# Performance work log

Measured on AMD Instinct MI355X. Metric: run time of the kernel, lower is better.

The kernel has to match this reference:

```python
import jax, jax.numpy as jnp
import numpy as np

TEMPERATURE = 0.07
MARGIN = 0.2
EPS = 1e-8  # matches torch F.cosine_similarity eps


def _cosine_matrix(a, b):
    # a: (N, D), b: (M, D) -> (N, M) pairwise cosine similarity
    an = a / jnp.clip(jnp.linalg.norm(a, axis=-1, keepdims=True), EPS)
    bn = b / jnp.clip(jnp.linalg.norm(b, axis=-1, keepdims=True), EPS)
    return an @ bn.T


def setup_inputs() -> dict:
    key = jax.random.key(0)
    k1, k2, k3 = jax.random.split(key, 3)
    return {
        "step_embeddings": jax.random.normal(k1, (8192, 1024), dtype=jnp.float32),
        "modal_embeddings": jax.random.normal(k2, (4096, 1024), dtype=jnp.float32),
        "negative_modal_embeddings": jax.random.normal(k3, (4096, 1024), dtype=jnp.float32),
    }


def reference(step_embeddings, modal_embeddings, negative_modal_embeddings):
    # --- step-modal alignment (max cosine sim per step, averaged) ---
    S = _cosine_matrix(step_embeddings, modal_embeddings)        # (N, M)
    per_step = S.max(axis=1)                                      # (N,)
    alignment = per_step.mean()

    # --- attention-weighted alignment (use_attention=True) ---
    logits = (step_embeddings @ modal_embeddings.T) / TEMPERATURE  # (N, M)
    attention = jax.nn.softmax(logits, axis=1)
    weighted_alignment = (S * attention).sum(axis=1).mean()

    # --- contrastive coherence against negatives ---
    Sn = _cosine_matrix(step_embeddings, negative_modal_embeddings)
    negative_alignment = Sn.max(axis=1).mean()
    positive_alignment = alignment
    contrastive_score = positive_alignment - negative_alignment
    margin_score = jax.nn.relu(contrastive_score - MARGIN)

    # --- per-step coherence (same max-cosine per step) ---
    min_step_coherence = per_step.min()

    # overall uses weighted_alignment (attention on), mixed with contrastive
    overall = 0.7 * weighted_alignment + 0.3 * contrastive_score

    return (alignment, weighted_alignment, attention, contrastive_score,
            margin_score, positive_alignment, negative_alignment,
            per_step, min_step_coherence, overall)
```

## Files before the change

### kernel.cpp

```cpp
#include <hip/hip_runtime.h>
#include <cmath>


#define WAVE 64

typedef __bf16 bf16x8_t __attribute__((ext_vector_type(8)));
typedef __bf16 bf16x4_t __attribute__((ext_vector_type(4)));
typedef float f32x4_t __attribute__((ext_vector_type(4)));

__device__ __forceinline__ float wave_reduce_sum(float v) {
#pragma unroll
    for (int o = 32; o > 0; o >>= 1) v += __shfl_down(v, o, WAVE);
    return v;
}
__device__ __forceinline__ float wave_reduce_max(float v) {
#pragma unroll
    for (int o = 32; o > 0; o >>= 1) v = fmaxf(v, __shfl_down(v, o, WAVE));
    return v;
}
__device__ __forceinline__ float wave_reduce_min(float v) {
#pragma unroll
    for (int o = 32; o > 0; o >>= 1) v = fminf(v, __shfl_down(v, o, WAVE));
    return v;
}

__device__ __forceinline__ unsigned enc_f(float f) {
    unsigned u = __float_as_uint(f);
    return (u & 0x80000000u) ? ~u : (u | 0x80000000u);
}
__device__ __forceinline__ float dec_f(unsigned e) {
    unsigned u = (e & 0x80000000u) ? (e & 0x7fffffffu) : ~e;
    return __uint_as_float(u);
}

__global__ __launch_bounds__(256)
void convert_norms_kernel(const float* __restrict__ step,
                          const float* __restrict__ modal,
                          const float* __restrict__ negs,
                          char* __restrict__ arena,
                          float* __restrict__ ina, float* __restrict__ inb,
                          float* __restrict__ inn,
                          unsigned* __restrict__ negmax_u, int N, int M) {
    const int tid = threadIdx.x, lane = tid & 63, wv = tid >> 6;
    const int b = blockIdx.x * 4 + wv;
    const float* src;
    if (b < N)          src = step  + (size_t)b * 1024;
    else if (b < N + M) src = modal + (size_t)(b - N) * 1024;
    else                src = negs  + (size_t)(b - N - M) * 1024;

    char* cb = arena + (((size_t)(b >> 2)) << 14) + ((size_t)(b & 3) << 11) + 8192;
    float s = 0.0f;
#pragma unroll
    for (int q = 0; q < 4; q++) {
        const int idx = lane + q * 64;
        const float4 v = ((const float4*)src)[idx];
        bf16x4_t o;
        o[0] = (__bf16)v.x; o[1] = (__bf16)v.y;
        o[2] = (__bf16)v.z; o[3] = (__bf16)v.w;
        *(bf16x4_t*)(cb + (size_t)idx * 8) = o;
        s += v.x * v.x + v.y * v.y + v.z * v.z + v.w * v.w;
    }
    s = wave_reduce_sum(s);
    if (lane == 0) {
        const float inv = 1.0f / fmaxf(sqrtf(s), 1e-8f);
        if (b < N)          { ina[b] = inv; negmax_u[b] = 0u; }
        else if (b < N + M) inb[b - N] = inv;
        else                inn[b - N - M] = inv;
    }
}

#define GLD16(g, l)                                                       \
    __builtin_amdgcn_global_load_lds(                                     \
        (const __attribute__((address_space(1))) void*)(g),               \
        (__attribute__((address_space(3))) void*)(l), 16, 0, 0)

#define BAR()   asm volatile("s_barrier" ::: "memory")
#define LGKM0() asm volatile("s_waitcnt lgkmcnt(0)" ::: "memory")
#define VMW(n)  asm volatile("s_waitcnt vmcnt(" #n ")" ::: "memory")

#define STAGE_A(Ab, kt)                                                   \
    _Pragma("unroll")                                                     \
    for (int h = 0; h < 2; h++)                                           \
    _Pragma("unroll")                                                     \
      for (int c = 0; c < 2; c++)                                         \
        GLD16(arena + srcA[h][c] + (size_t)(kt) * 128,                    \
              (Ab) + h * 8192 + c * 4096 + w * 512);

#define STAGE_B(Bb, kt)                                                   \
    _Pragma("unroll")                                                     \
    for (int h = 0; h < 2; h++)                                           \
    _Pragma("unroll")                                                     \
      for (int c = 0; c < 2; c++)                                         \
        GLD16(arena + srcB[h][c] + (size_t)(kt) * 128,                    \
              (Bb) + h * 8192 + c * 4096 + w * 512);

#define READ_A(g, Ab)                                                     \
    _Pragma("unroll")                                                     \
    for (int ii = 0; ii < 4; ii++)                                        \
    _Pragma("unroll")                                                     \
      for (int kk = 0; kk < 2; kk++)                                      \
        af[ii][kk] = *(const bf16x8_t*)&(Ab)[arow0 + (g) * 4096 +         \
                                             ii * 1024 + koff[kk]];

#define READ_B(j0, dst, Bb)                                               \
    _Pragma("unroll")                                                     \
    for (int jj = 0; jj < 2; jj++)                                        \
    _Pragma("unroll")                                                     \
      for (int kk = 0; kk < 2; kk++)                                      \
        dst[jj][kk] = *(const bf16x8_t*)&(Bb)[brow0 + ((j0) + jj) * 1024 +\
                                              koff[kk]];

#define READ_B01(Bb) READ_B(0, bf01, Bb)
#define READ_B23(Bb) READ_B(2, bf23, Bb)

#define MFMA_Q(i0, j0, bsrc)                                              \
    __builtin_amdgcn_s_setprio(1);                                        \
    _Pragma("unroll")                                                     \
    for (int kk = 0; kk < 2; kk++)                                        \
    _Pragma("unroll")                                                     \
      for (int ii = 0; ii < 4; ii++)                                      \
      _Pragma("unroll")                                                   \
        for (int jj = 0; jj < 2; jj++)                                    \
          acc[(i0) + ii][(j0) + jj] =                                     \
              __builtin_amdgcn_mfma_f32_16x16x32_bf16(                    \
                  af[ii][kk], bsrc[jj][kk], acc[(i0) + ii][(j0) + jj],    \
                  0, 0, 0);                                               \
    __builtin_amdgcn_s_setprio(0);

#define TILE(Ac, Bc, An, Bn, ktpre, pre, rd)                              \
    LGKM0();                     \
    MFMA_Q(0, 0, bf01);                                                   \
    READ_B23(Bc);                           \
    LGKM0();                                                              \
    MFMA_Q(0, 2, bf23);                                                   \
    READ_A(1, Ac);          \
    BAR();                        \
    if (pre) { STAGE_B(Bc, ktpre); }                                      \
    LGKM0();                                             \
    MFMA_Q(4, 0, bf01);                                                   \
    BAR();                        \
    if (pre) { STAGE_A(Ac, ktpre); }                                      \
    MFMA_Q(4, 2, bf23);                                                   \
    if (rd) {                                                             \
        if (pre) { VMW(8); } else { VMW(0); }                             \
        BAR();                      \
        READ_A(0, An);           \
        READ_B01(Bn);                                                     \
    }

__global__ __launch_bounds__(512, 2)
void gemm_fused_kernel(char* __restrict__ arena, int N, int M,
                       const float* __restrict__ inv_nn,
                       unsigned* __restrict__ negmax_u) {
    __shared__ __bf16 As[2][256 * 64];
    __shared__ __bf16 Bs[2][256 * 64];

    const int lin = blockIdx.x;
    const int xcd = lin & 7;
    const int j   = lin >> 3;
    const int r   = j >> 5;
    const int u   = j & 31;
    const int bm = ((xcd << 2) + (u & 3)) << 8;
    const int bn = ((r << 3) + (u >> 2)) << 8;

    const int t = threadIdx.x, w = t >> 6, lane = t & 63;
    const int lane16 = lane & 15, lq = lane >> 4;
    const int wm = w >> 2, wn = w & 3;

    const int l3 = lane >> 3, ol = lane & 7;
    const int og = ol ^ l3;
    unsigned srcA[2][2], srcB[2][2];
#pragma unroll
    for (int h = 0; h < 2; h++)
#pragma unroll
      for (int c = 0; c < 2; c++) {
        const int ga = bm + h * 128 + c * 64 + w * 8 + l3;
        srcA[h][c] = ((unsigned)(ga >> 2) << 14) + ((unsigned)(ga & 3) << 11)
                     + 8192u + (unsigned)og * 16u;
        const int gb = N + bn + h * 128 + c * 64 + w * 8 + l3;
        srcB[h][c] = ((unsigned)(gb >> 2) << 14) + ((unsigned)(gb & 3) << 11)
                     + 8192u + (unsigned)og * 16u;
      }

    const int sxr = lane16 & 7;
    int koff[2];
#pragma unroll
    for (int kk = 0; kk < 2; kk++) koff[kk] = ((lq + 4 * kk) ^ sxr) * 8;
    const int arow0 = wm * 8192 + lane16 * 64;
    const int brow0 = wn * 4096 + lane16 * 64;

    f32x4_t acc[8][4];
#pragma unroll
    for (int i = 0; i < 8; i++)
#pragma unroll
      for (int j2 = 0; j2 < 4; j2++) acc[i][j2] = (f32x4_t){0.f, 0.f, 0.f, 0.f};

    bf16x8_t af[4][2], bf01[2][2], bf23[2][2];

    __bf16* const A0 = As[0]; __bf16* const A1 = As[1];
    __bf16* const B0 = Bs[0]; __bf16* const B1 = Bs[1];

    STAGE_A(A0, 0); STAGE_B(B0, 0);
    STAGE_A(A1, 1); STAGE_B(B1, 1);
    VMW(8);
    BAR();
    READ_A(0, A0);
    READ_B01(B0);

    for (int it = 0; it < 8; ++it) {
        const int pre = (it < 7);
        const int k2 = 2 * it + 2, k3 = 2 * it + 3;
        TILE(A0, B0, A1, B1, k2, pre, 1)
        TILE(A1, B1, A0, B0, k3, pre, pre)
    }

    if (bn < M) {
#pragma unroll
        for (int i = 0; i < 8; i++) {
#pragma unroll
            for (int rr = 0; rr < 4; rr++) {
                const int grow = bm + wm * 128 + i * 16 + lq * 4 + rr;
                __bf16* dst = (__bf16*)(arena + ((size_t)grow << 14)) +
                              bn + wn * 64 + lane16;
#pragma unroll
                for (int jj = 0; jj < 4; jj++)
                    dst[jj * 16] = (__bf16)acc[i][jj][rr];
            }
        }
    } else {
        float invn[4];
#pragma unroll
        for (int jj = 0; jj < 4; jj++)
            invn[jj] = inv_nn[(bn - M) + wn * 64 + jj * 16 + lane16];
#pragma unroll
        for (int i = 0; i < 8; i++) {
#pragma unroll
            for (int rr = 0; rr < 4; rr++) {
                float v = acc[i][0][rr] * invn[0];
                v = fmaxf(v, acc[i][1][rr] * invn[1]);
                v = fmaxf(v, acc[i][2][rr] * invn[2]);
                v = fmaxf(v, acc[i][3][rr] * invn[3]);
#pragma unroll
                for (int o = 8; o > 0; o >>= 1)
                    v = fmaxf(v, __shfl_xor(v, o, WAVE));
                if (lane16 == 0)
                    atomicMax(&negmax_u[bm + wm * 128 + i * 16 + lq * 4 + rr],
                              enc_f(v));
            }
        }
    }
}

#define CUT 2.0f
#define MAXCAND 64

__global__ __launch_bounds__(256)
void softmax_fix_kernel(char* __restrict__ arena, const float* __restrict__ step,
                        const float* __restrict__ modal,
                        const float* __restrict__ ina, const float* __restrict__ inb,
                        float* __restrict__ perstep, float* __restrict__ wout,
                        float* __restrict__ attn) {
    const int row = blockIdx.x, tid = threadIdx.x;
    const int lane = tid & 63, wv = tid >> 6;

    __shared__ float srow_s[1024];
    __shared__ float red[8];
    __shared__ float bcast[2];
    __shared__ int   cand[MAXCAND];
    __shared__ float exact[MAXCAND];
    __shared__ int   cnt;

    if (tid == 0) cnt = 0;
    ((float4*)srow_s)[tid] = ((const float4*)(step + (size_t)row * 1024))[tid];

    const __bf16* gb = (const __bf16*)(arena + ((size_t)row << 14));
    float vals[16];
    float invn[16];
#pragma unroll
    for (int g = 0; g < 4; g++) {
        const bf16x4_t v = *(const bf16x4_t*)(gb + g * 1024 + tid * 4);
        const float4 x = *(const float4*)(inb + g * 1024 + tid * 4);
        vals[g * 4 + 0] = (float)v[0]; vals[g * 4 + 1] = (float)v[1];
        vals[g * 4 + 2] = (float)v[2]; vals[g * 4 + 3] = (float)v[3];
        invn[g * 4 + 0] = x.x; invn[g * 4 + 1] = x.y;
        invn[g * 4 + 2] = x.z; invn[g * 4 + 3] = x.w;
    }

    float dmax = -3.4e38f;
#pragma unroll
    for (int j = 0; j < 16; j++) dmax = fmaxf(dmax, vals[j]);
    float wm = wave_reduce_max(dmax);
    if (lane == 0) red[wv] = wm;
    __syncthreads();
    if (tid == 0) bcast[0] = fmaxf(fmaxf(red[0], red[1]), fmaxf(red[2], red[3]));
    __syncthreads();
    const float m0 = bcast[0];

    const float thr = m0 - CUT;
#pragma unroll
    for (int g = 0; g < 4; g++)
#pragma unroll
        for (int u = 0; u < 4; u++) {
            if (vals[g * 4 + u] >= thr) {
                const int pos = atomicAdd(&cnt, 1);
                if (pos < MAXCAND) cand[pos] = g * 1024 + tid * 4 + u;
            }
        }
    __syncthreads();
    const int nc = min(cnt, MAXCAND);

    for (int i = wv; i < nc; i += 4) {
        const float* mrow = modal + (size_t)cand[i] * 1024;
        float p = 0.0f;
#pragma unroll
        for (int q = 0; q < 16; q++) {
            const int idx = lane + q * 64;
            p = fmaf(srow_s[idx], mrow[idx], p);
        }
        p = wave_reduce_sum(p);
        if (lane == 0) exact[i] = p;
    }
    __syncthreads();

    for (int i = 0; i < nc; i++) {
        const int c = cand[i];
        if (((c & 1023) >> 2) == tid) vals[(c >> 10) * 4 + (c & 3)] = exact[i];
    }

    float dmax2 = -3.4e38f, cmax = -3.4e38f;
#pragma unroll
    for (int j = 0; j < 16; j++) {
        dmax2 = fmaxf(dmax2, vals[j]);
        cmax = fmaxf(cmax, vals[j] * invn[j]);
    }
    float wg = wave_reduce_max(dmax2);
    float wc = wave_reduce_max(cmax);
    if (lane == 0) { red[wv] = wg; red[4 + wv] = wc; }
    __syncthreads();
    if (tid == 0) {
        bcast[0] = fmaxf(fmaxf(red[0], red[1]), fmaxf(red[2], red[3]));
        bcast[1] = fmaxf(fmaxf(red[4], red[5]), fmaxf(red[6], red[7]));
    }
    __syncthreads();
    const float invT = 1.0f / 0.07f;
    const float mlog = bcast[0] * invT;
    const float cmaxAll = bcast[1];

    float evals[16];
    float lsum = 0.0f;
#pragma unroll
    for (int j = 0; j < 16; j++) {
        const float e = __expf(vals[j] * invT - mlog);
        evals[j] = e;
        lsum += e;
    }
    lsum = wave_reduce_sum(lsum);
    __syncthreads();
    if (lane == 0) red[wv] = lsum;
    __syncthreads();
    if (tid == 0) bcast[0] = red[0] + red[1] + red[2] + red[3];
    __syncthreads();
    const float invZ = 1.0f / bcast[0];

    float* arow = attn + (size_t)row * 4096;
    float wacc = 0.0f;
#pragma unroll
    for (int g = 0; g < 4; g++) {
        float4 o;
        const float a0 = evals[g * 4 + 0] * invZ, a1 = evals[g * 4 + 1] * invZ;
        const float a2 = evals[g * 4 + 2] * invZ, a3 = evals[g * 4 + 3] * invZ;
        o.x = a0; o.y = a1; o.z = a2; o.w = a3;
        *(float4*)(arow + g * 1024 + tid * 4) = o;
        wacc += a0 * vals[g * 4 + 0] * invn[g * 4 + 0];
        wacc += a1 * vals[g * 4 + 1] * invn[g * 4 + 1];
        wacc += a2 * vals[g * 4 + 2] * invn[g * 4 + 2];
        wacc += a3 * vals[g * 4 + 3] * invn[g * 4 + 3];
    }
    wacc = wave_reduce_sum(wacc);
    __syncthreads();
    if (lane == 0) red[wv] = wacc;
    __syncthreads();
    if (tid == 0) {
        const float inv_na = ina[row];
        perstep[row] = cmaxAll * inv_na;
        wout[row] = (red[0] + red[1] + red[2] + red[3]) * inv_na;
    }
}

__global__ __launch_bounds__(1024)
void finalize_kernel(const float* __restrict__ perstep, const float* __restrict__ w,
                     const unsigned* __restrict__ negmax_u,
                     const float* __restrict__ ina, float* __restrict__ out,
                     int N, size_t NM) {
    float s_a = 0.0f, s_w = 0.0f, s_n = 0.0f, mn = 3.4e38f;
    for (int i = threadIdx.x; i < N; i += 1024) {
        const float p = perstep[i];
        s_a += p;
        s_w += w[i];
        s_n += dec_f(negmax_u[i]) * ina[i];
        mn = fminf(mn, p);
    }
    s_a = wave_reduce_sum(s_a);
    s_w = wave_reduce_sum(s_w);
    s_n = wave_reduce_sum(s_n);
    mn  = wave_reduce_min(mn);
    __shared__ float ra[16], rw[16], rn[16], rm[16];
    const int lane = threadIdx.x & 63, wv = threadIdx.x >> 6;
    if (lane == 0) { ra[wv] = s_a; rw[wv] = s_w; rn[wv] = s_n; rm[wv] = mn; }
    __syncthreads();
    if (threadIdx.x == 0) {
        float ta = 0, tw = 0, tn = 0, tm = 3.4e38f;
#pragma unroll
        for (int i = 0; i < 16; i++) {
            ta += ra[i]; tw += rw[i]; tn += rn[i]; tm = fminf(tm, rm[i]);
        }
        const float inv = 1.0f / (float)N;
        const float alignment = ta * inv;
        const float weighted  = tw * inv;
        const float neg       = tn * inv;
        const float contrast  = alignment - neg;
        const float margin    = fmaxf(contrast - 0.2f, 0.0f);
        const float overall   = 0.7f * weighted + 0.3f * contrast;
        out[0] = alignment;
        out[1] = weighted;
        float* p = out + 2 + NM;
        p[0] = contrast;
        p[1] = margin;
        p[2] = alignment;
        p[3] = neg;
        p[4 + N] = tm;
        p[5 + N] = overall;
    }
}

extern "C" void kernel_launch(void* const* d_in, const int* in_sizes, int n_in,
                              void* d_out, int out_size, void* d_ws, size_t ws_size,
                              hipStream_t stream) {
    const float* step  = (const float*)d_in[0];
    const float* modal = (const float*)d_in[1];
    const float* negs  = (const float*)d_in[2];
    float* out = (float*)d_out;

    const int K = 1024;
    const int N = in_sizes[0] / K;
    const int M = in_sizes[1] / K;
    const size_t NM = (size_t)N * (size_t)M;

    float* ina        = (float*)d_ws;
    float* inb        = ina + N;
    float* inn        = inb + M;
    unsigned* negmax  = (unsigned*)(inn + M);
    float* wsum       = (float*)(negmax + N);

    char* arena    = (char*)d_out + 16;
    float* attn    = out + 2;
    float* perstep = out + 2 + NM + 4;

    convert_norms_kernel<<<(N + 2 * M) / 4, 256, 0, stream>>>(
        step, modal, negs, arena, ina, inb, inn, negmax, N, M);

    const int nblocks = (N >> 8) * ((2 * M) >> 8);
    gemm_fused_kernel<<<nblocks, 512, 0, stream>>>(arena, N, M, inn, negmax);

    softmax_fix_kernel<<<N, 256, 0, stream>>>(arena, step, modal, ina, inb,
                                              perstep, wsum, attn);

    finalize_kernel<<<1, 1024, 0, stream>>>(perstep, wsum, negmax, ina, out, N, NM);
}
```

Measured before the change: 353.2 us.

## Reshape GEMM warp tiling to 64x128 and pipeline B fragment reads per quarter

Changes the per-wave output tile from 128x64 (2x4 wave grid) to 64x128 (4x2 grid), so each wave holds a single A fragment set and streams four B column chunks. The inner tile now double-buffers the B fragments with partial lgkmcnt waits and scheduling barriers so LDS reads overlap MFMAs. Global-to-LDS staging for the next k-tile is moved to after all MFMAs, between two barriers. The goal is fewer A fragment reloads and better overlap of LDS reads with compute, but the k-tile prefetch is now issued later, which leaves less time to hide global load latency.

```diff
diff --git a/kernel.cpp b/kernel.cpp
--- a/kernel.cpp
+++ b/kernel.cpp
@@ -74,9 +74,10 @@
         (const __attribute__((address_space(1))) void*)(g),               \
         (__attribute__((address_space(3))) void*)(l), 16, 0, 0)
 
-#define BAR()   asm volatile("s_barrier" ::: "memory")
-#define LGKM0() asm volatile("s_waitcnt lgkmcnt(0)" ::: "memory")
-#define VMW(n)  asm volatile("s_waitcnt vmcnt(" #n ")" ::: "memory")
+#define BAR()     asm volatile("s_barrier" ::: "memory")
+#define LGKMC(n)  asm volatile("s_waitcnt lgkmcnt(" #n ")" ::: "memory")
+#define VMW(n)    asm volatile("s_waitcnt vmcnt(" #n ")" ::: "memory")
+#define SB0()     __builtin_amdgcn_sched_barrier(0)
 
 #define STAGE_A(Ab, kt)                                                   \
     _Pragma("unroll")                                                     \
@@ -94,26 +95,23 @@
         GLD16(arena + srcB[h][c] + (size_t)(kt) * 128,                    \
               (Bb) + h * 8192 + c * 4096 + w * 512);
 
-#define READ_A(g, Ab)                                                     \
+#define READ_AF(Ab)                                                       \
     _Pragma("unroll")                                                     \
     for (int ii = 0; ii < 4; ii++)                                        \
     _Pragma("unroll")                                                     \
       for (int kk = 0; kk < 2; kk++)                                      \
-        af[ii][kk] = *(const bf16x8_t*)&(Ab)[arow0 + (g) * 4096 +         \
-                                             ii * 1024 + koff[kk]];
-
-#define READ_B(j0, dst, Bb)                                               \
+        af[ii][kk] = *(const bf16x8_t*)&(Ab)[arow0 + ii * 1024 +          \
+                                             koff[kk]];
+
+#define READ_BF(dst, c, Bb)                                               \
     _Pragma("unroll")                                                     \
     for (int jj = 0; jj < 2; jj++)                                        \
     _Pragma("unroll")                                                     \
       for (int kk = 0; kk < 2; kk++)                                      \
-        dst[jj][kk] = *(const bf16x8_t*)&(Bb)[brow0 + ((j0) + jj) * 1024 +\
-                                              koff[kk]];
-
-#define READ_B01(Bb) READ_B(0, bf01, Bb)
-#define READ_B23(Bb) READ_B(2, bf23, Bb)
-
-#define MFMA_Q(i0, j0, bsrc)                                              \
+        dst[jj][kk] = *(const bf16x8_t*)&(Bb)[brow0 + (c) * 2048 +        \
+                                              jj * 1024 + koff[kk]];
+
+#define MFMA_Q(c, bank)                                                   \
     __builtin_amdgcn_s_setprio(1);                                        \
     _Pragma("unroll")                                                     \
     for (int kk = 0; kk < 2; kk++)                                        \
@@ -121,31 +119,31 @@
       for (int ii = 0; ii < 4; ii++)                                      \
       _Pragma("unroll")                                                   \
         for (int jj = 0; jj < 2; jj++)                                    \
-          acc[(i0) + ii][(j0) + jj] =                                     \
+          acc[ii][(c) * 2 + jj] =                                         \
               __builtin_amdgcn_mfma_f32_16x16x32_bf16(                    \
-                  af[ii][kk], bsrc[jj][kk], acc[(i0) + ii][(j0) + jj],    \
+                  af[ii][kk], bank[jj][kk], acc[ii][(c) * 2 + jj],        \
                   0, 0, 0);                                               \
     __builtin_amdgcn_s_setprio(0);
 
 #define TILE(Ac, Bc, An, Bn, ktpre, pre, rd)                              \
-    LGKM0();                     \
-    MFMA_Q(0, 0, bf01);                                                   \
-    READ_B23(Bc);                           \
-    LGKM0();                                                              \
-    MFMA_Q(0, 2, bf23);                                                   \
-    READ_A(1, Ac);          \
-    BAR();                        \
-    if (pre) { STAGE_B(Bc, ktpre); }                                      \
-    LGKM0();                                             \
-    MFMA_Q(4, 0, bf01);                                                   \
-    BAR();                        \
-    if (pre) { STAGE_A(Ac, ktpre); }                                      \
-    MFMA_Q(4, 2, bf23);                                                   \
+    READ_BF(bfO, 1, Bc);                                                  \
+    LGKMC(4); SB0();                      \
+    MFMA_Q(0, bfE);                                                       \
+    READ_BF(bfE, 2, Bc);                                                  \
+    LGKMC(4); SB0();                         \
+    MFMA_Q(1, bfO);                                                       \
+    READ_BF(bfO, 3, Bc);                                                  \
+    LGKMC(4); SB0();                         \
+    MFMA_Q(2, bfE);                                                       \
+    LGKMC(0); SB0();                                        \
+    MFMA_Q(3, bfO);                                                       \
     if (rd) {                                                             \
-        if (pre) { VMW(8); } else { VMW(0); }                             \
-        BAR();                      \
-        READ_A(0, An);           \
-        READ_B01(Bn);                                                     \
+        BAR();                       \
+        if (pre) { STAGE_A(Ac, ktpre); STAGE_B(Bc, ktpre); VMW(8); }      \
+        else     { VMW(0); }                                              \
+        BAR();                                    \
+        READ_AF(An);                \
+        READ_BF(bfE, 0, Bn);                                              \
     }
 
 __global__ __launch_bounds__(512, 2)
@@ -165,7 +163,7 @@
 
     const int t = threadIdx.x, w = t >> 6, lane = t & 63;
     const int lane16 = lane & 15, lq = lane >> 4;
-    const int wm = w >> 2, wn = w & 3;
+    const int wm = w & 3, wn = w >> 2;
 
     const int l3 = lane >> 3, ol = lane & 7;
     const int og = ol ^ l3;
@@ -186,16 +184,16 @@
     int koff[2];
 #pragma unroll
     for (int kk = 0; kk < 2; kk++) koff[kk] = ((lq + 4 * kk) ^ sxr) * 8;
-    const int arow0 = wm * 8192 + lane16 * 64;
-    const int brow0 = wn * 4096 + lane16 * 64;
-
-    f32x4_t acc[8][4];
-#pragma unroll
-    for (int i = 0; i < 8; i++)
-#pragma unroll
-      for (int j2 = 0; j2 < 4; j2++) acc[i][j2] = (f32x4_t){0.f, 0.f, 0.f, 0.f};
-
-    bf16x8_t af[4][2], bf01[2][2], bf23[2][2];
+    const int arow0 = wm * 4096 + lane16 * 64;
+    const int brow0 = wn * 8192 + lane16 * 64;
+
+    f32x4_t acc[4][8];
+#pragma unroll
+    for (int i = 0; i < 4; i++)
+#pragma unroll
+      for (int j2 = 0; j2 < 8; j2++) acc[i][j2] = (f32x4_t){0.f, 0.f, 0.f, 0.f};
+
+    bf16x8_t af[4][2], bfE[2][2], bfO[2][2];
 
     __bf16* const A0 = As[0]; __bf16* const A1 = As[1];
     __bf16* const B0 = Bs[0]; __bf16* const B1 = Bs[1];
@@ -204,8 +202,8 @@
     STAGE_A(A1, 1); STAGE_B(B1, 1);
     VMW(8);
     BAR();
-    READ_A(0, A0);
-    READ_B01(B0);
+    READ_AF(A0);
+    READ_BF(bfE, 0, B0);
 
     for (int it = 0; it < 8; ++it) {
         const int pre = (it < 7);
@@ -216,35 +214,35 @@
 
     if (bn < M) {
 #pragma unroll
-        for (int i = 0; i < 8; i++) {
+        for (int i = 0; i < 4; i++) {
 #pragma unroll
             for (int rr = 0; rr < 4; rr++) {
-                const int grow = bm + wm * 128 + i * 16 + lq * 4 + rr;
+                const int grow = bm + wm * 64 + i * 16 + lq * 4 + rr;
                 __bf16* dst = (__bf16*)(arena + ((size_t)grow << 14)) +
-                              bn + wn * 64 + lane16;
-#pragma unroll
-                for (int jj = 0; jj < 4; jj++)
+                              bn + wn * 128 + lane16;
+#pragma unroll
+                for (int jj = 0; jj < 8; jj++)
                     dst[jj * 16] = (__bf16)acc[i][jj][rr];
             }
         }
     } else {
-        float invn[4];
-#pragma unroll
-        for (int jj = 0; jj < 4; jj++)
-            invn[jj] = inv_nn[(bn - M) + wn * 64 + jj * 16 + lane16];
-#pragma unroll
-        for (int i = 0; i < 8; i++) {
+        float invn[8];
+#pragma unroll
+        for (int jj = 0; jj < 8; jj++)
+            invn[jj] = inv_nn[(bn - M) + wn * 128 + jj * 16 + lane16];
+#pragma unroll
+        for (int i = 0; i < 4; i++) {
 #pragma unroll
             for (int rr = 0; rr < 4; rr++) {
                 float v = acc[i][0][rr] * invn[0];
-                v = fmaxf(v, acc[i][1][rr] * invn[1]);
-                v = fmaxf(v, acc[i][2][rr] * invn[2]);
-                v = fmaxf(v, acc[i][3][rr] * invn[3]);
+#pragma unroll
+                for (int jj = 1; jj < 8; jj++)
+                    v = fmaxf(v, acc[i][jj][rr] * invn[jj]);
 #pragma unroll
                 for (int o = 8; o > 0; o >>= 1)
                     v = fmaxf(v, __shfl_xor(v, o, WAVE));
                 if (lane16 == 0)
-                    atomicMax(&negmax_u[bm + wm * 128 + i * 16 + lq * 4 + rr],
+                    atomicMax(&negmax_u[bm + wm * 64 + i * 16 + lq * 4 + rr],
                               enc_f(v));
             }
         }
```

New measurement: 366.5 us. +3.8%, slower.
